# Kernel tuning notes

Hardware: AMD Instinct MI355X
Metric: run time of the kernel (lower is better)

The kernel has to match this reference:

```python
import jax, jax.numpy as jnp
import numpy as np

D_MODEL = 256
NHEAD = 8
DHEAD = D_MODEL // NHEAD
LN_EPS = 1e-5
ATTN_EPS = 1e-6


def layer_norm(x, gamma, beta):
    mu = jnp.mean(x, axis=-1, keepdims=True)
    var = jnp.mean(jnp.square(x - mu), axis=-1, keepdims=True)
    return (x - mu) * jax.lax.rsqrt(var + LN_EPS) * gamma + beta


def setup_inputs() -> dict:
    key = jax.random.key(0)
    ks = jax.random.split(key, 12)
    B, L, S = 8, 4096, 4096
    s = 1.0 / np.sqrt(D_MODEL)
    return {
        "x": jax.random.normal(ks[0], (B, L, D_MODEL), jnp.float32),
        "source": jax.random.normal(ks[1], (B, S, D_MODEL), jnp.float32),
        "wq": jax.random.normal(ks[2], (D_MODEL, D_MODEL), jnp.float32) * s,
        "wk": jax.random.normal(ks[3], (D_MODEL, D_MODEL), jnp.float32) * s,
        "wv": jax.random.normal(ks[4], (D_MODEL, D_MODEL), jnp.float32) * s,
        "wmerge": jax.random.normal(ks[5], (D_MODEL, D_MODEL), jnp.float32) * s,
        "w1": jax.random.normal(ks[6], (2 * D_MODEL, D_MODEL), jnp.float32) * s,
        "w2": jax.random.normal(ks[7], (D_MODEL, 2 * D_MODEL), jnp.float32) * (1.0 / np.sqrt(2 * D_MODEL)),
        "g1": jnp.ones((D_MODEL,), jnp.float32),
        "b1": jnp.zeros((D_MODEL,), jnp.float32),
        "g2": jnp.ones((D_MODEL,), jnp.float32),
        "b2": jnp.zeros((D_MODEL,), jnp.float32),
    }


def reference(x, source, wq, wk, wv, wmerge, w1, w2, g1, b1, g2, b2):
    B, L, _ = x.shape
    S = source.shape[1]
    # QKV projections (bias-free Linear: y = x @ W^T), split into heads
    q = (x @ wq.T).reshape(B, L, NHEAD, DHEAD)
    k = (source @ wk.T).reshape(B, S, NHEAD, DHEAD)
    v = (source @ wv.T).reshape(B, S, NHEAD, DHEAD)
    # LinearAttention (LoFTR): feature map elu(.)+1, kernelized attention
    Q = jax.nn.elu(q) + 1.0
    K = jax.nn.elu(k) + 1.0
    v_len = jnp.asarray(S, v.dtype)
    values = v / v_len
    KV = jnp.einsum('bshd,bshv->bhdv', K, values)        # [B,H,D,D]
    Z = 1.0 / (jnp.einsum('blhd,bhd->blh', Q, K.sum(axis=1)) + ATTN_EPS)
    attended = jnp.einsum('blhd,bhdv,blh->blhv', Q, KV, Z) * v_len
    # merge + residual LN
    message = attended.reshape(B, L, D_MODEL) @ wmerge.T
    x = x + layer_norm(message, g1, b1)
    # MLP (d -> 2d -> d, ReLU) + residual LN
    h = jax.nn.relu(x @ w1.T) @ w2.T
    x = x + layer_norm(h, g2, b2)
    return x
```

## Files before the change

kernel.cpp:

```cpp
#include <hip/hip_runtime.h>

#define DM 256
#define SEQ 4096

typedef __attribute__((ext_vector_type(8))) short bf16x8;
typedef __attribute__((ext_vector_type(4))) float f32x4;

#define MFMA16(a, b, c) __builtin_amdgcn_mfma_f32_16x16x32_bf16(a, b, c, 0, 0, 0)

__device__ __forceinline__ short f2bf(float f) {
    union { float f; unsigned u; } c; c.f = f;
    unsigned r = (c.u + 0x7FFFu + ((c.u >> 16) & 1u)) >> 16;
    return (short)r;
}
__device__ __forceinline__ float bf2f(short s) {
    union { unsigned u; float f; } c; c.u = ((unsigned)(unsigned short)s) << 16; return c.f;
}
__device__ __forceinline__ bf16x8 pack8(float4 a, float4 b) {
    bf16x8 r;
    r[0] = f2bf(a.x); r[1] = f2bf(a.y); r[2] = f2bf(a.z); r[3] = f2bf(a.w);
    r[4] = f2bf(b.x); r[5] = f2bf(b.y); r[6] = f2bf(b.z); r[7] = f2bf(b.w);
    return r;
}

__global__ __launch_bounds__(256) void kWconv(const float* __restrict__ wq, const float* __restrict__ wk,
                                              const float* __restrict__ wv, const float* __restrict__ wm,
                                              const float* __restrict__ w1, const float* __restrict__ w2,
                                              short* __restrict__ dstws) {
    int blk = blockIdx.x;
    const float* src; short* dst;
    if (blk < 32)       { src = wq; dst = dstws;          }
    else if (blk < 64)  { src = wk; dst = dstws + 65536;  blk -= 32; }
    else if (blk < 96)  { src = wv; dst = dstws + 131072; blk -= 64; }
    else if (blk < 128) { src = wm; dst = dstws + 196608; blk -= 96; }
    else if (blk < 192) { src = w1; dst = dstws + 262144; blk -= 128; }
    else                { src = w2; dst = dstws + 393216; blk -= 192; }
    int idx = (blk * 256 + threadIdx.x) * 8;
    float4 f0 = *(const float4*)(src + idx), f1 = *(const float4*)(src + idx + 4);
    *(bf16x8*)(dst + idx) = pack8(f0, f1);
}

__global__ __launch_bounds__(512, 4) void kA(const float* __restrict__ src,
                                             const short* __restrict__ wk, const short* __restrict__ wv,
                                             float* __restrict__ kv_part, float* __restrict__ ksum_part) {
    __shared__ char lds[65536];
    int t = threadIdx.x, lane = t & 63, w = t >> 6, r16 = lane & 15, g = lane >> 4;
    int b = blockIdx.x >> 6, blk = blockIdx.x & 63;
    const float* S = src + ((size_t)b * SEQ + blk * 64) * DM;
#pragma unroll
    for (int i = 0; i < 4; i++) {
        int chunk = t + i * 512, row = chunk >> 5, c8 = chunk & 31;
        const float* p = S + row * DM + c8 * 8;
        float4 f0 = *(const float4*)p, f1 = *(const float4*)(p + 4);
        int by = (row * 512 + c8 * 16) ^ ((row & 7) << 4);
        *(bf16x8*)(lds + by) = pack8(f0, f1);
    }
    __syncthreads();
    f32x4 zz = {0.f, 0.f, 0.f, 0.f};
    f32x4 ak[4][2], av[4][2];
#pragma unroll
    for (int mi = 0; mi < 4; mi++)
#pragma unroll
        for (int ni = 0; ni < 2; ni++) { ak[mi][ni] = zz; av[mi][ni] = zz; }
#pragma unroll
    for (int kt = 0; kt < 8; kt++) {
        bf16x8 A[4];
#pragma unroll
        for (int mi = 0; mi < 4; mi++) {
            int row = mi * 16 + r16;
            A[mi] = *(const bf16x8*)(lds + ((row * 512 + (kt * 32 + g * 8) * 2) ^ ((row & 7) << 4)));
        }
#pragma unroll
        for (int ni = 0; ni < 2; ni++) {
            int n = w * 32 + ni * 16 + r16;
            bf16x8 Bk = *(const bf16x8*)(wk + n * DM + kt * 32 + g * 8);
            bf16x8 Bv = *(const bf16x8*)(wv + n * DM + kt * 32 + g * 8);
#pragma unroll
            for (int mi = 0; mi < 4; mi++) {
                ak[mi][ni] = MFMA16(A[mi], Bk, ak[mi][ni]);
                av[mi][ni] = MFMA16(A[mi], Bv, av[mi][ni]);
            }
        }
    }
    __syncthreads();
    char* kT = lds + w * 8192;
    char* vT = kT + 4096;
    float ksp[2] = {0.f, 0.f};
#pragma unroll
    for (int mi = 0; mi < 4; mi++)
#pragma unroll
        for (int ni = 0; ni < 2; ni++)
#pragma unroll
            for (int j = 0; j < 4; j++) {
                float q = ak[mi][ni][j];
                float e = q > 0.f ? q + 1.f : __expf(q);
                ksp[ni] += e;
                int srow = mi * 16 + g * 4 + j, feat = ni * 16 + r16;
                int by = (feat * 128 + srow * 2) ^ ((feat & 7) << 4);
                *(short*)(kT + by) = f2bf(e);
                *(short*)(vT + by) = f2bf(av[mi][ni][j]);
            }
    __syncthreads();
    f32x4 kv[2][2];
#pragma unroll
    for (int vi = 0; vi < 2; vi++)
#pragma unroll
        for (int di = 0; di < 2; di++) kv[vi][di] = zz;
#pragma unroll
    for (int st = 0; st < 2; st++) {
        bf16x8 Af[2], Bf[2];
#pragma unroll
        for (int vi = 0; vi < 2; vi++) {
            int row = vi * 16 + r16;
            Af[vi] = *(const bf16x8*)(vT + ((row * 128 + (st * 32 + g * 8) * 2) ^ ((row & 7) << 4)));
            Bf[vi] = *(const bf16x8*)(kT + ((row * 128 + (st * 32 + g * 8) * 2) ^ ((row & 7) << 4)));
        }
#pragma unroll
        for (int vi = 0; vi < 2; vi++)
#pragma unroll
            for (int di = 0; di < 2; di++) kv[vi][di] = MFMA16(Af[vi], Bf[di], kv[vi][di]);
    }
    float* kvp = kv_part + ((size_t)(b * 64 + blk) * 8 + w) * 1024;
#pragma unroll
    for (int vi = 0; vi < 2; vi++)
#pragma unroll
        for (int di = 0; di < 2; di++)
#pragma unroll
            for (int j = 0; j < 4; j++) {
                int v = vi * 16 + g * 4 + j, d = di * 16 + r16;
                kvp[v * 32 + d] = kv[vi][di][j];
            }
#pragma unroll
    for (int ni = 0; ni < 2; ni++) {
        ksp[ni] += __shfl_xor(ksp[ni], 16);
        ksp[ni] += __shfl_xor(ksp[ni], 32);
    }
    if (lane < 16) {
        float* kp = ksum_part + (size_t)(b * 64 + blk) * 256 + w * 32;
#pragma unroll
        for (int ni = 0; ni < 2; ni++) kp[ni * 16 + lane] = ksp[ni];
    }
}

__global__ __launch_bounds__(256) void kA2(const float* __restrict__ kv_part, const float* __restrict__ ksum_part,
                                           short* __restrict__ kvt_bf, float* __restrict__ ksum) {
    int blk = blockIdx.x, t = threadIdx.x;
    int b = blk >> 5, h = (blk >> 2) & 7, q = blk & 3;
    int e = q * 256 + t;
    float s0 = 0.f, s1 = 0.f, s2 = 0.f, s3 = 0.f;
    for (int bk = 0; bk < 64; bk += 4) {
        s0 += kv_part[((size_t)(b * 64 + bk) * 8 + h) * 1024 + e];
        s1 += kv_part[((size_t)(b * 64 + bk + 1) * 8 + h) * 1024 + e];
        s2 += kv_part[((size_t)(b * 64 + bk + 2) * 8 + h) * 1024 + e];
        s3 += kv_part[((size_t)(b * 64 + bk + 3) * 8 + h) * 1024 + e];
    }
    kvt_bf[(size_t)(b * 8 + h) * 1024 + e] = f2bf((s0 + s1) + (s2 + s3));
    if (q == 3 && t < 32) {
        float s = 0.f;
        for (int bk = 0; bk < 64; bk++)
            s += ksum_part[(size_t)(b * 64 + bk) * 256 + h * 32 + t];
        ksum[(b * 8 + h) * 32 + t] = s;
    }
}

__global__ __launch_bounds__(512, 4) void kBC(const float* __restrict__ x,
                                              const short* __restrict__ wq_bf, const short* __restrict__ wm_bf,
                                              const short* __restrict__ w1_bf, const short* __restrict__ w2_bf,
                                              const short* __restrict__ kvt_bf, const float* __restrict__ ksum,
                                              const float* __restrict__ g1, const float* __restrict__ b1,
                                              const float* __restrict__ g2, const float* __restrict__ b2,
                                              float* __restrict__ out) {
    __shared__ char lds[52224];
    char* xt = lds;
    char* hb = lds + 16384;
    char* qa = lds + 16384;
    float* red = (float*)(lds + 49152);
    float* ksl = (float*)(lds + 51200);
    int t = threadIdx.x, lane = t & 63, w = t >> 6, r16 = lane & 15, g = lane >> 4;
    int b = blockIdx.x >> 7, lb = blockIdx.x & 127, l0 = lb * 32;
    const float* xb = x + ((size_t)b * SEQ + l0) * DM;
#pragma unroll
    for (int i = 0; i < 2; i++) {
        int chunk = t + i * 512, row = chunk >> 5, c8 = chunk & 31;
        const float* p = xb + row * DM + c8 * 8;
        float4 f0 = *(const float4*)p, f1 = *(const float4*)(p + 4);
        int by = (row * 512 + c8 * 16) ^ ((row & 7) << 4);
        *(bf16x8*)(xt + by) = pack8(f0, f1);
    }
    if (t < 256) ksl[t] = ksum[b * 256 + t];
    __syncthreads();
    f32x4 zz = {0.f, 0.f, 0.f, 0.f};
    f32x4 acc[2][2];
#pragma unroll
    for (int mi = 0; mi < 2; mi++)
#pragma unroll
        for (int ni = 0; ni < 2; ni++) acc[mi][ni] = zz;
#pragma unroll
    for (int kt = 0; kt < 8; kt++) {
        bf16x8 A[2], Bf[2];
#pragma unroll
        for (int mi = 0; mi < 2; mi++) {
            int row = mi * 16 + r16;
            A[mi] = *(const bf16x8*)(xt + ((row * 512 + (kt * 32 + g * 8) * 2) ^ ((row & 7) << 4)));
        }
#pragma unroll
        for (int ni = 0; ni < 2; ni++)
            Bf[ni] = *(const bf16x8*)(wq_bf + (w * 32 + ni * 16 + r16) * DM + kt * 32 + g * 8);
#pragma unroll
        for (int mi = 0; mi < 2; mi++)
#pragma unroll
            for (int ni = 0; ni < 2; ni++) acc[mi][ni] = MFMA16(A[mi], Bf[ni], acc[mi][ni]);
    }
    float ks0 = ksl[w * 32 + r16], ks1 = ksl[w * 32 + 16 + r16];
    float Zr[2][4];
#pragma unroll
    for (int mi = 0; mi < 2; mi++)
#pragma unroll
        for (int j = 0; j < 4; j++) {
#pragma unroll
            for (int ni = 0; ni < 2; ni++) {
                float q = acc[mi][ni][j];
                acc[mi][ni][j] = q > 0.f ? q + 1.f : __expf(q);
            }
            float d0 = acc[mi][0][j] * ks0 + acc[mi][1][j] * ks1;
#pragma unroll
            for (int m = 1; m < 16; m <<= 1) d0 += __shfl_xor(d0, m);
            Zr[mi][j] = 1.f / (d0 + 1e-6f);
        }
#pragma unroll
    for (int mi = 0; mi < 2; mi++)
#pragma unroll
        for (int ni = 0; ni < 2; ni++)
#pragma unroll
            for (int j = 0; j < 4; j++) {
                int row = mi * 16 + g * 4 + j, col = w * 32 + ni * 16 + r16;
                *(short*)(qa + ((row * 512 + col * 2) ^ ((row & 7) << 4))) = f2bf(acc[mi][ni][j]);
            }
    f32x4 at[2][2];
#pragma unroll
    for (int mi = 0; mi < 2; mi++)
#pragma unroll
        for (int vi = 0; vi < 2; vi++) at[mi][vi] = zz;
    {
        bf16x8 A2[2], B2[2];
#pragma unroll
        for (int mi = 0; mi < 2; mi++) {
            int row = mi * 16 + r16, col = w * 32 + g * 8;
            A2[mi] = *(const bf16x8*)(qa + ((row * 512 + col * 2) ^ ((row & 7) << 4)));
        }
        const short* kvb = kvt_bf + (size_t)(b * 8 + w) * 1024;
#pragma unroll
        for (int vi = 0; vi < 2; vi++)
            B2[vi] = *(const bf16x8*)(kvb + (vi * 16 + r16) * 32 + g * 8);
#pragma unroll
        for (int mi = 0; mi < 2; mi++)
#pragma unroll
            for (int vi = 0; vi < 2; vi++) at[mi][vi] = MFMA16(A2[mi], B2[vi], at[mi][vi]);
    }
#pragma unroll
    for (int mi = 0; mi < 2; mi++)
#pragma unroll
        for (int vi = 0; vi < 2; vi++)
#pragma unroll
            for (int j = 0; j < 4; j++) {
                int row = mi * 16 + g * 4 + j, col = w * 32 + vi * 16 + r16;
                *(short*)(qa + ((row * 512 + col * 2) ^ ((row & 7) << 4))) = f2bf(at[mi][vi][j] * Zr[mi][j]);
            }
    __syncthreads();
    f32x4 am[2][2];
#pragma unroll
    for (int mi = 0; mi < 2; mi++)
#pragma unroll
        for (int ni = 0; ni < 2; ni++) am[mi][ni] = zz;
#pragma unroll
    for (int kt = 0; kt < 8; kt++) {
        bf16x8 A[2], Bf[2];
#pragma unroll
        for (int mi = 0; mi < 2; mi++) {
            int row = mi * 16 + r16;
            A[mi] = *(const bf16x8*)(qa + ((row * 512 + (kt * 32 + g * 8) * 2) ^ ((row & 7) << 4)));
        }
#pragma unroll
        for (int ni = 0; ni < 2; ni++)
            Bf[ni] = *(const bf16x8*)(wm_bf + (w * 32 + ni * 16 + r16) * DM + kt * 32 + g * 8);
#pragma unroll
        for (int mi = 0; mi < 2; mi++)
#pragma unroll
            for (int ni = 0; ni < 2; ni++) am[mi][ni] = MFMA16(A[mi], Bf[ni], am[mi][ni]);
    }
#pragma unroll
    for (int mi = 0; mi < 2; mi++)
#pragma unroll
        for (int j = 0; j < 4; j++) {
            float s = am[mi][0][j] + am[mi][1][j];
            float s2 = am[mi][0][j] * am[mi][0][j] + am[mi][1][j] * am[mi][1][j];
#pragma unroll
            for (int m = 1; m < 16; m <<= 1) { s += __shfl_xor(s, m); s2 += __shfl_xor(s2, m); }
            if (r16 == 0) { int row = mi * 16 + g * 4 + j; red[(row * 8 + w) * 2] = s; red[(row * 8 + w) * 2 + 1] = s2; }
        }
    __syncthreads();
    {
        float g1v[2], b1v[2];
#pragma unroll
        for (int ni = 0; ni < 2; ni++) { int col = w * 32 + ni * 16 + r16; g1v[ni] = g1[col]; b1v[ni] = b1[col]; }
#pragma unroll
        for (int mi = 0; mi < 2; mi++)
#pragma unroll
            for (int j = 0; j < 4; j++) {
                int row = mi * 16 + g * 4 + j;
                float mu = 0.f, ex2 = 0.f;
#pragma unroll
                for (int ww = 0; ww < 8; ww++) { mu += red[(row * 8 + ww) * 2]; ex2 += red[(row * 8 + ww) * 2 + 1]; }
                mu *= (1.f / DM); ex2 *= (1.f / DM);
                float rstd = rsqrtf(ex2 - mu * mu + 1e-5f);
#pragma unroll
                for (int ni = 0; ni < 2; ni++) {
                    int col = w * 32 + ni * 16 + r16;
                    int by = (row * 512 + col * 2) ^ ((row & 7) << 4);
                    float xv = bf2f(*(const short*)(xt + by));
                    *(short*)(xt + by) = f2bf(xv + (am[mi][ni][j] - mu) * rstd * g1v[ni] + b1v[ni]);
                }
            }
    }
    __syncthreads();
    f32x4 a1[2][4];
#pragma unroll
    for (int mi = 0; mi < 2; mi++)
#pragma unroll
        for (int ni = 0; ni < 4; ni++) a1[mi][ni] = zz;
#pragma unroll
    for (int kt = 0; kt < 8; kt++) {
        bf16x8 A[2], Bf[4];
#pragma unroll
        for (int mi = 0; mi < 2; mi++) {
            int row = mi * 16 + r16;
            A[mi] = *(const bf16x8*)(xt + ((row * 512 + (kt * 32 + g * 8) * 2) ^ ((row & 7) << 4)));
        }
#pragma unroll
        for (int ni = 0; ni < 4; ni++)
            Bf[ni] = *(const bf16x8*)(w1_bf + (w * 64 + ni * 16 + r16) * DM + kt * 32 + g * 8);
#pragma unroll
        for (int mi = 0; mi < 2; mi++)
#pragma unroll
            for (int ni = 0; ni < 4; ni++) a1[mi][ni] = MFMA16(A[mi], Bf[ni], a1[mi][ni]);
    }
#pragma unroll
    for (int mi = 0; mi < 2; mi++)
#pragma unroll
        for (int ni = 0; ni < 4; ni++)
#pragma unroll
            for (int j = 0; j < 4; j++) {
                float hv = a1[mi][ni][j]; hv = hv > 0.f ? hv : 0.f;
                int row = mi * 16 + g * 4 + j, col = w * 64 + ni * 16 + r16;
                *(short*)(hb + ((row * 1024 + col * 2) ^ ((row & 7) << 4))) = f2bf(hv);
            }
    __syncthreads();
    f32x4 a2[2][2];
#pragma unroll
    for (int mi = 0; mi < 2; mi++)
#pragma unroll
        for (int ni = 0; ni < 2; ni++) a2[mi][ni] = zz;
#pragma unroll
    for (int kt = 0; kt < 16; kt++) {
        bf16x8 A[2], Bf[2];
#pragma unroll
        for (int mi = 0; mi < 2; mi++) {
            int row = mi * 16 + r16;
            A[mi] = *(const bf16x8*)(hb + ((row * 1024 + (kt * 32 + g * 8) * 2) ^ ((row & 7) << 4)));
        }
#pragma unroll
        for (int ni = 0; ni < 2; ni++)
            Bf[ni] = *(const bf16x8*)(w2_bf + (w * 32 + ni * 16 + r16) * 512 + kt * 32 + g * 8);
#pragma unroll
        for (int mi = 0; mi < 2; mi++)
#pragma unroll
            for (int ni = 0; ni < 2; ni++) a2[mi][ni] = MFMA16(A[mi], Bf[ni], a2[mi][ni]);
    }
#pragma unroll
    for (int mi = 0; mi < 2; mi++)
#pragma unroll
        for (int j = 0; j < 4; j++) {
            float s = a2[mi][0][j] + a2[mi][1][j];
            float s2 = a2[mi][0][j] * a2[mi][0][j] + a2[mi][1][j] * a2[mi][1][j];
#pragma unroll
            for (int m = 1; m < 16; m <<= 1) { s += __shfl_xor(s, m); s2 += __shfl_xor(s2, m); }
            if (r16 == 0) { int row = mi * 16 + g * 4 + j; red[(row * 8 + w) * 2] = s; red[(row * 8 + w) * 2 + 1] = s2; }
        }
    __syncthreads();
    {
        float g2v[2], b2v[2];
#pragma unroll
        for (int ni = 0; ni < 2; ni++) { int col = w * 32 + ni * 16 + r16; g2v[ni] = g2[col]; b2v[ni] = b2[col]; }
        float* op = out + ((size_t)b * SEQ + l0) * DM;
#pragma unroll
        for (int mi = 0; mi < 2; mi++)
#pragma unroll
            for (int j = 0; j < 4; j++) {
                int row = mi * 16 + g * 4 + j;
                float mu = 0.f, ex2 = 0.f;
#pragma unroll
                for (int ww = 0; ww < 8; ww++) { mu += red[(row * 8 + ww) * 2]; ex2 += red[(row * 8 + ww) * 2 + 1]; }
                mu *= (1.f / DM); ex2 *= (1.f / DM);
                float rstd = rsqrtf(ex2 - mu * mu + 1e-5f);
#pragma unroll
                for (int ni = 0; ni < 2; ni++) {
                    int col = w * 32 + ni * 16 + r16;
                    float xv = bf2f(*(const short*)(xt + ((row * 512 + col * 2) ^ ((row & 7) << 4))));
                    op[row * DM + col] = xv + (a2[mi][ni][j] - mu) * rstd * g2v[ni] + b2v[ni];
                }
            }
    }
}

extern "C" void kernel_launch(void* const* d_in, const int* in_sizes, int n_in,
                              void* d_out, int out_size, void* d_ws, size_t ws_size,
                              hipStream_t stream) {
    const float* x   = (const float*)d_in[0];
    const float* src = (const float*)d_in[1];
    const float* wq  = (const float*)d_in[2];
    const float* wk  = (const float*)d_in[3];
    const float* wv  = (const float*)d_in[4];
    const float* wm  = (const float*)d_in[5];
    const float* w1  = (const float*)d_in[6];
    const float* w2  = (const float*)d_in[7];
    const float* g1  = (const float*)d_in[8];
    const float* b1  = (const float*)d_in[9];
    const float* g2  = (const float*)d_in[10];
    const float* b2  = (const float*)d_in[11];
    float* out = (float*)d_out;

    char* ws = (char*)d_ws;
    short* w_bf      = (short*)ws;
    short* kvt_bf    = (short*)(ws + 1048576);
    float* ksum      = (float*)(ws + 1179648);
    float* kv_part   = (float*)(ws + 1187840);
    float* ksum_part = (float*)(ws + 17965056);

    kWconv<<<256, 256, 0, stream>>>(wq, wk, wv, wm, w1, w2, w_bf);
    kA<<<512, 512, 0, stream>>>(src, w_bf + 65536, w_bf + 131072, kv_part, ksum_part);
    kA2<<<256, 256, 0, stream>>>(kv_part, ksum_part, kvt_bf, ksum);
    kBC<<<1024, 512, 0, stream>>>(x, w_bf, w_bf + 196608, w_bf + 262144, w_bf + 393216,
                                  kvt_bf, ksum, g1, b1, g2, b2, out);
}
```

Before: 247.7 us.

## Halve tiles and LDS in kA/kBC, store KV partials in bf16, split MLP hidden

kA now processes 32 source rows per block over twice as many blocks, using half the LDS and raising the launch-bound occupancy target to 8. It writes its KV partials as bf16 instead of fp32, which halves the partial traffic but adds rounding before the reduction. The ksum reduction is spread over all four kA2 quarter-blocks, and kBC adds the four pieces. kBC's MLP computes the 512-wide hidden layer in two 256-wide halves that reuse the qa buffer, shrinking LDS and register use at the cost of extra barriers.

New measurement: 302.3 us. +22.0%, slower.

```diff
diff --git a/kernel.cpp b/kernel.cpp
--- a/kernel.cpp
+++ b/kernel.cpp
@@ -40,15 +40,15 @@
     *(bf16x8*)(dst + idx) = pack8(f0, f1);
 }
 
-__global__ __launch_bounds__(512, 4) void kA(const float* __restrict__ src,
+__global__ __launch_bounds__(512, 8) void kA(const float* __restrict__ src,
                                              const short* __restrict__ wk, const short* __restrict__ wv,
-                                             float* __restrict__ kv_part, float* __restrict__ ksum_part) {
-    __shared__ char lds[65536];
+                                             short* __restrict__ kv_part, float* __restrict__ ksum_part) {
+    __shared__ char lds[32768];
     int t = threadIdx.x, lane = t & 63, w = t >> 6, r16 = lane & 15, g = lane >> 4;
-    int b = blockIdx.x >> 6, blk = blockIdx.x & 63;
-    const float* S = src + ((size_t)b * SEQ + blk * 64) * DM;
-#pragma unroll
-    for (int i = 0; i < 4; i++) {
+    int b = blockIdx.x >> 7, blk = blockIdx.x & 127;
+    const float* S = src + ((size_t)b * SEQ + blk * 32) * DM;
+#pragma unroll
+    for (int i = 0; i < 2; i++) {
         int chunk = t + i * 512, row = chunk >> 5, c8 = chunk & 31;
         const float* p = S + row * DM + c8 * 8;
         float4 f0 = *(const float4*)p, f1 = *(const float4*)(p + 4);
@@ -57,16 +57,16 @@
     }
     __syncthreads();
     f32x4 zz = {0.f, 0.f, 0.f, 0.f};
-    f32x4 ak[4][2], av[4][2];
-#pragma unroll
-    for (int mi = 0; mi < 4; mi++)
+    f32x4 ak[2][2], av[2][2];
+#pragma unroll
+    for (int mi = 0; mi < 2; mi++)
 #pragma unroll
         for (int ni = 0; ni < 2; ni++) { ak[mi][ni] = zz; av[mi][ni] = zz; }
 #pragma unroll
     for (int kt = 0; kt < 8; kt++) {
-        bf16x8 A[4];
-#pragma unroll
-        for (int mi = 0; mi < 4; mi++) {
+        bf16x8 A[2];
+#pragma unroll
+        for (int mi = 0; mi < 2; mi++) {
             int row = mi * 16 + r16;
             A[mi] = *(const bf16x8*)(lds + ((row * 512 + (kt * 32 + g * 8) * 2) ^ ((row & 7) << 4)));
         }
@@ -76,18 +76,18 @@
             bf16x8 Bk = *(const bf16x8*)(wk + n * DM + kt * 32 + g * 8);
             bf16x8 Bv = *(const bf16x8*)(wv + n * DM + kt * 32 + g * 8);
 #pragma unroll
-            for (int mi = 0; mi < 4; mi++) {
+            for (int mi = 0; mi < 2; mi++) {
                 ak[mi][ni] = MFMA16(A[mi], Bk, ak[mi][ni]);
                 av[mi][ni] = MFMA16(A[mi], Bv, av[mi][ni]);
             }
         }
     }
     __syncthreads();
-    char* kT = lds + w * 8192;
-    char* vT = kT + 4096;
+    char* kT = lds + w * 4096;
+    char* vT = kT + 2048;
     float ksp[2] = {0.f, 0.f};
 #pragma unroll
-    for (int mi = 0; mi < 4; mi++)
+    for (int mi = 0; mi < 2; mi++)
 #pragma unroll
         for (int ni = 0; ni < 2; ni++)
 #pragma unroll
@@ -96,7 +96,7 @@
                 float e = q > 0.f ? q + 1.f : __expf(q);
                 ksp[ni] += e;
                 int srow = mi * 16 + g * 4 + j, feat = ni * 16 + r16;
-                int by = (feat * 128 + srow * 2) ^ ((feat & 7) << 4);
+                int by = feat * 64 + srow * 2;
                 *(short*)(kT + by) = f2bf(e);
                 *(short*)(vT + by) = f2bf(av[mi][ni][j]);
             }
@@ -106,21 +106,20 @@
     for (int vi = 0; vi < 2; vi++)
 #pragma unroll
         for (int di = 0; di < 2; di++) kv[vi][di] = zz;
-#pragma unroll
-    for (int st = 0; st < 2; st++) {
+    {
         bf16x8 Af[2], Bf[2];
 #pragma unroll
         for (int vi = 0; vi < 2; vi++) {
             int row = vi * 16 + r16;
-            Af[vi] = *(const bf16x8*)(vT + ((row * 128 + (st * 32 + g * 8) * 2) ^ ((row & 7) << 4)));
-            Bf[vi] = *(const bf16x8*)(kT + ((row * 128 + (st * 32 + g * 8) * 2) ^ ((row & 7) << 4)));
+            Af[vi] = *(const bf16x8*)(vT + row * 64 + g * 16);
+            Bf[vi] = *(const bf16x8*)(kT + row * 64 + g * 16);
         }
 #pragma unroll
         for (int vi = 0; vi < 2; vi++)
 #pragma unroll
             for (int di = 0; di < 2; di++) kv[vi][di] = MFMA16(Af[vi], Bf[di], kv[vi][di]);
     }
-    float* kvp = kv_part + ((size_t)(b * 64 + blk) * 8 + w) * 1024;
+    short* kvp = kv_part + ((size_t)(b * 128 + blk) * 8 + w) * 1024;
 #pragma unroll
     for (int vi = 0; vi < 2; vi++)
 #pragma unroll
@@ -128,7 +127,7 @@
 #pragma unroll
             for (int j = 0; j < 4; j++) {
                 int v = vi * 16 + g * 4 + j, d = di * 16 + r16;
-                kvp[v * 32 + d] = kv[vi][di][j];
+                kvp[v * 32 + d] = f2bf(kv[vi][di][j]);
             }
 #pragma unroll
     for (int ni = 0; ni < 2; ni++) {
@@ -136,46 +135,45 @@
         ksp[ni] += __shfl_xor(ksp[ni], 32);
     }
     if (lane < 16) {
-        float* kp = ksum_part + (size_t)(b * 64 + blk) * 256 + w * 32;
+        float* kp = ksum_part + (size_t)(b * 128 + blk) * 256 + w * 32;
 #pragma unroll
         for (int ni = 0; ni < 2; ni++) kp[ni * 16 + lane] = ksp[ni];
     }
 }
 
-__global__ __launch_bounds__(256) void kA2(const float* __restrict__ kv_part, const float* __restrict__ ksum_part,
-                                           short* __restrict__ kvt_bf, float* __restrict__ ksum) {
+__global__ __launch_bounds__(256) void kA2(const short* __restrict__ kv_part, const float* __restrict__ ksum_part,
+                                           short* __restrict__ kvt_bf, float* __restrict__ ksum4) {
     int blk = blockIdx.x, t = threadIdx.x;
     int b = blk >> 5, h = (blk >> 2) & 7, q = blk & 3;
     int e = q * 256 + t;
     float s0 = 0.f, s1 = 0.f, s2 = 0.f, s3 = 0.f;
-    for (int bk = 0; bk < 64; bk += 4) {
-        s0 += kv_part[((size_t)(b * 64 + bk) * 8 + h) * 1024 + e];
-        s1 += kv_part[((size_t)(b * 64 + bk + 1) * 8 + h) * 1024 + e];
-        s2 += kv_part[((size_t)(b * 64 + bk + 2) * 8 + h) * 1024 + e];
-        s3 += kv_part[((size_t)(b * 64 + bk + 3) * 8 + h) * 1024 + e];
+    for (int bk = 0; bk < 128; bk += 4) {
+        s0 += bf2f(kv_part[((size_t)(b * 128 + bk) * 8 + h) * 1024 + e]);
+        s1 += bf2f(kv_part[((size_t)(b * 128 + bk + 1) * 8 + h) * 1024 + e]);
+        s2 += bf2f(kv_part[((size_t)(b * 128 + bk + 2) * 8 + h) * 1024 + e]);
+        s3 += bf2f(kv_part[((size_t)(b * 128 + bk + 3) * 8 + h) * 1024 + e]);
     }
     kvt_bf[(size_t)(b * 8 + h) * 1024 + e] = f2bf((s0 + s1) + (s2 + s3));
-    if (q == 3 && t < 32) {
+    if (t < 32) {
         float s = 0.f;
-        for (int bk = 0; bk < 64; bk++)
-            s += ksum_part[(size_t)(b * 64 + bk) * 256 + h * 32 + t];
-        ksum[(b * 8 + h) * 32 + t] = s;
-    }
-}
-
-__global__ __launch_bounds__(512, 4) void kBC(const float* __restrict__ x,
+        for (int bk = q * 32; bk < q * 32 + 32; bk++)
+            s += ksum_part[(size_t)(b * 128 + bk) * 256 + h * 32 + t];
+        ksum4[((b * 8 + h) * 4 + q) * 32 + t] = s;
+    }
+}
+
+__global__ __launch_bounds__(512, 8) void kBC(const float* __restrict__ x,
                                               const short* __restrict__ wq_bf, const short* __restrict__ wm_bf,
                                               const short* __restrict__ w1_bf, const short* __restrict__ w2_bf,
-                                              const short* __restrict__ kvt_bf, const float* __restrict__ ksum,
+                                              const short* __restrict__ kvt_bf, const float* __restrict__ ksum4,
                                               const float* __restrict__ g1, const float* __restrict__ b1,
                                               const float* __restrict__ g2, const float* __restrict__ b2,
                                               float* __restrict__ out) {
-    __shared__ char lds[52224];
+    __shared__ char lds[35840];
     char* xt = lds;
-    char* hb = lds + 16384;
     char* qa = lds + 16384;
-    float* red = (float*)(lds + 49152);
-    float* ksl = (float*)(lds + 51200);
+    float* red = (float*)(lds + 32768);
+    float* ksl = (float*)(lds + 34816);
     int t = threadIdx.x, lane = t & 63, w = t >> 6, r16 = lane & 15, g = lane >> 4;
     int b = blockIdx.x >> 7, lb = blockIdx.x & 127, l0 = lb * 32;
     const float* xb = x + ((size_t)b * SEQ + l0) * DM;
@@ -187,7 +185,11 @@
         int by = (row * 512 + c8 * 16) ^ ((row & 7) << 4);
         *(bf16x8*)(xt + by) = pack8(f0, f1);
     }
-    if (t < 256) ksl[t] = ksum[b * 256 + t];
+    if (t < 256) {
+        int h = t >> 5, d = t & 31;
+        const float* kp = ksum4 + (size_t)((b * 8 + h) * 4) * 32 + d;
+        ksl[t] = (kp[0] + kp[32]) + (kp[64] + kp[96]);
+    }
     __syncthreads();
     f32x4 zz = {0.f, 0.f, 0.f, 0.f};
     f32x4 acc[2][2];
@@ -323,58 +325,62 @@
             }
     }
     __syncthreads();
-    f32x4 a1[2][4];
-#pragma unroll
-    for (int mi = 0; mi < 2; mi++)
-#pragma unroll
-        for (int ni = 0; ni < 4; ni++) a1[mi][ni] = zz;
-#pragma unroll
-    for (int kt = 0; kt < 8; kt++) {
-        bf16x8 A[2], Bf[4];
-#pragma unroll
-        for (int mi = 0; mi < 2; mi++) {
-            int row = mi * 16 + r16;
-            A[mi] = *(const bf16x8*)(xt + ((row * 512 + (kt * 32 + g * 8) * 2) ^ ((row & 7) << 4)));
-        }
-#pragma unroll
-        for (int ni = 0; ni < 4; ni++)
-            Bf[ni] = *(const bf16x8*)(w1_bf + (w * 64 + ni * 16 + r16) * DM + kt * 32 + g * 8);
-#pragma unroll
-        for (int mi = 0; mi < 2; mi++)
-#pragma unroll
-            for (int ni = 0; ni < 4; ni++) a1[mi][ni] = MFMA16(A[mi], Bf[ni], a1[mi][ni]);
-    }
-#pragma unroll
-    for (int mi = 0; mi < 2; mi++)
-#pragma unroll
-        for (int ni = 0; ni < 4; ni++)
-#pragma unroll
-            for (int j = 0; j < 4; j++) {
-                float hv = a1[mi][ni][j]; hv = hv > 0.f ? hv : 0.f;
-                int row = mi * 16 + g * 4 + j, col = w * 64 + ni * 16 + r16;
-                *(short*)(hb + ((row * 1024 + col * 2) ^ ((row & 7) << 4))) = f2bf(hv);
-            }
-    __syncthreads();
     f32x4 a2[2][2];
 #pragma unroll
     for (int mi = 0; mi < 2; mi++)
 #pragma unroll
         for (int ni = 0; ni < 2; ni++) a2[mi][ni] = zz;
 #pragma unroll
-    for (int kt = 0; kt < 16; kt++) {
-        bf16x8 A[2], Bf[2];
-#pragma unroll
-        for (int mi = 0; mi < 2; mi++) {
-            int row = mi * 16 + r16;
-            A[mi] = *(const bf16x8*)(hb + ((row * 1024 + (kt * 32 + g * 8) * 2) ^ ((row & 7) << 4)));
-        }
-#pragma unroll
-        for (int ni = 0; ni < 2; ni++)
-            Bf[ni] = *(const bf16x8*)(w2_bf + (w * 32 + ni * 16 + r16) * 512 + kt * 32 + g * 8);
-#pragma unroll
-        for (int mi = 0; mi < 2; mi++)
-#pragma unroll
-            for (int ni = 0; ni < 2; ni++) a2[mi][ni] = MFMA16(A[mi], Bf[ni], a2[mi][ni]);
+    for (int hf = 0; hf < 2; hf++) {
+        f32x4 a1[2][2];
+#pragma unroll
+        for (int mi = 0; mi < 2; mi++)
+#pragma unroll
+            for (int ni = 0; ni < 2; ni++) a1[mi][ni] = zz;
+#pragma unroll
+        for (int kt = 0; kt < 8; kt++) {
+            bf16x8 A[2], Bf[2];
+#pragma unroll
+            for (int mi = 0; mi < 2; mi++) {
+                int row = mi * 16 + r16;
+                A[mi] = *(const bf16x8*)(xt + ((row * 512 + (kt * 32 + g * 8) * 2) ^ ((row & 7) << 4)));
+            }
+#pragma unroll
+            for (int ni = 0; ni < 2; ni++)
+                Bf[ni] = *(const bf16x8*)(w1_bf + (hf * 256 + w * 32 + ni * 16 + r16) * DM + kt * 32 + g * 8);
+#pragma unroll
+            for (int mi = 0; mi < 2; mi++)
+#pragma unroll
+                for (int ni = 0; ni < 2; ni++) a1[mi][ni] = MFMA16(A[mi], Bf[ni], a1[mi][ni]);
+        }
+#pragma unroll
+        for (int mi = 0; mi < 2; mi++)
+#pragma unroll
+            for (int ni = 0; ni < 2; ni++)
+#pragma unroll
+                for (int j = 0; j < 4; j++) {
+                    float hv = a1[mi][ni][j]; hv = hv > 0.f ? hv : 0.f;
+                    int row = mi * 16 + g * 4 + j, col = w * 32 + ni * 16 + r16;
+                    *(short*)(qa + ((row * 512 + col * 2) ^ ((row & 7) << 4))) = f2bf(hv);
+                }
+        __syncthreads();
+#pragma unroll
+        for (int kt = 0; kt < 8; kt++) {
+            bf16x8 A[2], Bf[2];
+#pragma unroll
+            for (int mi = 0; mi < 2; mi++) {
+                int row = mi * 16 + r16;
+                A[mi] = *(const bf16x8*)(qa + ((row * 512 + (kt * 32 + g * 8) * 2) ^ ((row & 7) << 4)));
+            }
+#pragma unroll
+            for (int ni = 0; ni < 2; ni++)
+                Bf[ni] = *(const bf16x8*)(w2_bf + (w * 32 + ni * 16 + r16) * 512 + hf * 256 + kt * 32 + g * 8);
+#pragma unroll
+            for (int mi = 0; mi < 2; mi++)
+#pragma unroll
+                for (int ni = 0; ni < 2; ni++) a2[mi][ni] = MFMA16(A[mi], Bf[ni], a2[mi][ni]);
+        }
+        __syncthreads();
     }
 #pragma unroll
     for (int mi = 0; mi < 2; mi++)
@@ -432,13 +438,13 @@
     char* ws = (char*)d_ws;
     short* w_bf      = (short*)ws;
     short* kvt_bf    = (short*)(ws + 1048576);
-    float* ksum      = (float*)(ws + 1179648);
-    float* kv_part   = (float*)(ws + 1187840);
-    float* ksum_part = (float*)(ws + 17965056);
+    float* ksum4     = (float*)(ws + 1179648);
+    short* kv_part   = (short*)(ws + 1212416);
+    float* ksum_part = (float*)(ws + 17989632);
 
     kWconv<<<256, 256, 0, stream>>>(wq, wk, wv, wm, w1, w2, w_bf);
-    kA<<<512, 512, 0, stream>>>(src, w_bf + 65536, w_bf + 131072, kv_part, ksum_part);
-    kA2<<<256, 256, 0, stream>>>(kv_part, ksum_part, kvt_bf, ksum);
+    kA<<<1024, 512, 0, stream>>>(src, w_bf + 65536, w_bf + 131072, kv_part, ksum_part);
+    kA2<<<256, 256, 0, stream>>>(kv_part, ksum_part, kvt_bf, ksum4);
     kBC<<<1024, 512, 0, stream>>>(x, w_bf, w_bf + 196608, w_bf + 262144, w_bf + 393216,
-                                  kvt_bf, ksum, g1, b1, g2, b2, out);
-}
+                                  kvt_bf, ksum4, g1, b1, g2, b2, out);
+}
```
